# Performance work log

Hardware: AMD Instinct MI355X
Metric: run time of the kernel (lower is better)

## Reference

```python
import jax, jax.numpy as jnp
import numpy as np

B, C, H, W = 2, 256, 128, 128
QK_DIM, HEADS, TOPK, NSP = 256, 8, 128, 256
HEAD_DIM = QK_DIM // HEADS
SCALE = HEAD_DIM ** -0.5
EPS = 1e-6


def setup_inputs() -> dict:
    key = jax.random.key(0)
    ks = jax.random.split(key, 5)
    return {
        "x": jax.random.normal(ks[0], (B, C, H, W), jnp.float32),
        "affinity_matrix": jax.random.normal(ks[1], (B, NSP, H * W), jnp.float32),
        "gamma": jnp.ones((C,), jnp.float32),
        "beta": jnp.zeros((C,), jnp.float32),
        "wq": jax.random.normal(ks[2], (QK_DIM, C), jnp.float32) * 0.02,
        "wk": jax.random.normal(ks[3], (QK_DIM, C), jnp.float32) * 0.02,
        "wv": jax.random.normal(ks[4], (C, C), jnp.float32) * 0.02,
        "num_spixels": NSP,
    }


def _split_heads(a, h):
    # [B, K, T, h*c] -> [B, K, h, T, c]   (channel layout is (h c), as in the torch rearrange)
    b, k, t, d = a.shape
    return a.reshape(b, k, t, h, d // h).transpose(0, 1, 3, 2, 4)


def _merge(a):
    # 'b k h t c -> b (h c) (k t)'
    b, k, h, t, c = a.shape
    return a.transpose(0, 2, 4, 1, 3).reshape(b, h * c, k * t)


def reference(x, affinity_matrix, gamma, beta, wq, wk, wv, num_spixels):
    # LayerNorm2d: normalize over channels with eps=1e-6
    xp = x.transpose(0, 2, 3, 1)                      # [B,H,W,C]
    mu = xp.mean(-1, keepdims=True)
    var = ((xp - mu) ** 2).mean(-1, keepdims=True)
    xn = (xp - mu) / jnp.sqrt(var + EPS) * gamma + beta
    xf = xn.reshape(B, H * W, C)                      # [B, HW, C]

    # 1x1 convs == per-pixel linear
    q = xf @ wq.T                                     # [B, HW, QK]
    k = xf @ wk.T                                     # [B, HW, QK]
    v = xf @ wv.T                                     # [B, HW, C]

    sims, idx = jax.lax.top_k(affinity_matrix, TOPK)  # [B, NSP, T]

    gather = jax.vmap(lambda feat, i: feat[i])        # [HW,D],[NSP,T] -> [NSP,T,D]
    qh = _split_heads(gather(q, idx), HEADS)          # [B,K,h,T,c]
    kh = _split_heads(gather(k, idx), HEADS)
    vh = _split_heads(gather(v, idx), HEADS)

    attn = jax.nn.softmax(jnp.einsum('bkhtc,bkhsc->bkhts', qh, kh) * SCALE, axis=-1)
    w = sims[:, :, None, :, None]                     # [B,K,1,T,1]
    out = jnp.einsum('bkhts,bkhsc->bkhtc', attn, w * vh)

    out_f = _merge(out)                               # [B, C, K*T]
    w_f = _merge(jnp.broadcast_to(w, vh.shape))       # [B, C, K*T]

    tgt = v.transpose(0, 2, 1)                        # [B, C, HW]
    idx_f = idx.reshape(B, -1)                        # [B, K*T]
    scat = jax.vmap(lambda t_, i_, s_: t_.at[:, i_].add(s_))
    res = scat(tgt, idx_f, w_f * out_f)               # scatter-add over pixels
    return res.reshape(B, C, H, W)
```

## Files before the change

### kernel.cpp

```cpp
#include <hip/hip_runtime.h>
#include <hip/hip_bf16.h>

#define B_ 2
#define C_ 256
#define H_ 128
#define W_ 128
#define HW_ 16384
#define QK_ 256
#define HEADS_ 8
#define HD_ 32
#define TOPK_ 128
#define NSP_ 256
#define SCALE_F 0.17677669529663687f
#define EPS_ 1e-6f

typedef __attribute__((ext_vector_type(16))) float f32x16;
typedef __attribute__((ext_vector_type(8))) short bf16x8;
typedef unsigned short ushort_t;
union FragU { unsigned int u[4]; bf16x8 v; };

__device__ __forceinline__ ushort_t f2bf(float x)
{
    unsigned u = __float_as_uint(x);
    return (ushort_t)((u + 0x7fffu + ((u >> 16) & 1u)) >> 16);
}
__device__ __forceinline__ float bf2f(ushort_t h)
{
    return __uint_as_float((unsigned)h << 16);
}
__device__ __forceinline__ unsigned pk2(float a, float b)
{
    return (unsigned)f2bf(a) | ((unsigned)f2bf(b) << 16);
}

__device__ __forceinline__ unsigned pk2n(float a, float b)
{
    __hip_bfloat162 h2 = __float22bfloat162_rn(make_float2(a, b));
    union { __hip_bfloat162 h; unsigned u; } c;
    c.h = h2;
    return c.u;
}

__device__ __forceinline__ void half_swap(unsigned a, unsigned b,
                                          unsigned& o0, unsigned& o1, int hi)
{
#if __has_builtin(__builtin_amdgcn_permlane32_swap)
    auto r = __builtin_amdgcn_permlane32_swap(a, b, false, false);
    o0 = (unsigned)r[0];
    o1 = (unsigned)r[1];
#else
    unsigned sa = (unsigned)__shfl_xor((int)a, 32);
    unsigned sb = (unsigned)__shfl_xor((int)b, 32);
    o0 = hi ? sb : a;
    o1 = hi ? b : sa;
#endif
}

__device__ __forceinline__ size_t frag_off(int panel, int ks, int lane)
{
    return (((size_t)panel * 16 + ks) * 64 + lane) * 8;
}

__device__ __forceinline__ void split8(const float* f, FragU& hi, FragU& lo)
{
    #pragma unroll
    for (int j = 0; j < 4; j++) {
        ushort_t h0 = f2bf(f[2*j]);
        ushort_t h1 = f2bf(f[2*j+1]);
        hi.u[j] = (unsigned)h0 | ((unsigned)h1 << 16);
        lo.u[j] = pk2(f[2*j] - bf2f(h0), f[2*j+1] - bf2f(h1));
    }
}

__global__ __launch_bounds__(256) void k_meanvar(const float* __restrict__ x, float* __restrict__ mu_rstd)
{
    int p = blockIdx.x * 256 + threadIdx.x;
    int b = p >> 14, pp = p & (HW_ - 1);
    const float* xb = x + (size_t)b * C_ * HW_ + pp;
    float s = 0.f, s2 = 0.f;
    for (int c = 0; c < C_; c++) {
        float v = xb[(size_t)c * HW_];
        s += v; s2 += v * v;
    }
    float mu = s * (1.f / C_);
    float var = s2 * (1.f / C_) - mu * mu;
    float rstd = rsqrtf(var + EPS_);
    mu_rstd[2 * p] = mu;
    mu_rstd[2 * p + 1] = rstd;
}

__global__ __launch_bounds__(256) void k_wsplit16(
    const float* __restrict__ wq, const float* __restrict__ wk, const float* __restrict__ wv,
    ushort_t* __restrict__ wf)
{
    const int panel = blockIdx.x;
    const int lm = threadIdx.x & 31;
    const int kg = threadIdx.x >> 5;
    const int k0 = kg * 32;
    const int n = panel * 32 + lm;
    const float* wr = (n < 256) ? (wq + (size_t)n * C_)
                   : (n < 512) ? (wk + (size_t)(n - 256) * C_)
                               : (wv + (size_t)(n - 512) * C_);
    float v[32];
    #pragma unroll
    for (int j4 = 0; j4 < 8; j4++) {
        float4 t = *(const float4*)(wr + k0 + j4 * 4);
        v[j4*4+0] = t.x; v[j4*4+1] = t.y; v[j4*4+2] = t.z; v[j4*4+3] = t.w;
    }
    uint4 hv[4];
    unsigned* hp = (unsigned*)hv;
    #pragma unroll
    for (int jp = 0; jp < 16; jp++)
        hp[jp] = pk2n(v[2*jp], v[2*jp+1]);
    #pragma unroll
    for (int q = 0; q < 4; q++) {
        const int kk = k0 + 8 * q;
        const int ks = kk >> 4;
        const int hi = (kk >> 3) & 1;
        *(uint4*)(wf + frag_off(panel, ks, lm + 32 * hi)) = hv[q];
    }
}

__global__ __launch_bounds__(256) void k_lnsplit16(
    const float* __restrict__ x, const float* __restrict__ gamma, const float* __restrict__ beta,
    ushort_t* __restrict__ xf)
{
    const int b = blockIdx.y;
    const int m0 = blockIdx.x * 32;
    const int lm = threadIdx.x & 31;
    const int kg = threadIdx.x >> 5;
    const int k0 = kg * 32;
    const int m = m0 + lm;
    const float* xb = x + (size_t)b * C_ * HW_ + m;
    __shared__ float g_l[C_], b_l[C_];
    __shared__ float red[2][8][32];
    g_l[threadIdx.x] = gamma[threadIdx.x];
    b_l[threadIdx.x] = beta[threadIdx.x];

    float v[32];
    float s = 0.f, s2 = 0.f;
    #pragma unroll
    for (int j = 0; j < 32; j++) {
        v[j] = xb[(size_t)(k0 + j) * HW_];
        s += v[j]; s2 += v[j] * v[j];
    }
    red[0][kg][lm] = s; red[1][kg][lm] = s2;
    __syncthreads();
    float ts = 0.f, ts2 = 0.f;
    #pragma unroll
    for (int g = 0; g < 8; g++) { ts += red[0][g][lm]; ts2 += red[1][g][lm]; }
    const float mu = ts * (1.f / C_);
    const float var = ts2 * (1.f / C_) - mu * mu;
    const float rstd = rsqrtf(var + EPS_);

    uint4 hv[4];
    unsigned* hp = (unsigned*)hv;
    #pragma unroll
    for (int jp = 0; jp < 16; jp++) {
        float l0 = (v[2*jp]   - mu) * rstd * g_l[k0 + 2*jp]   + b_l[k0 + 2*jp];
        float l1 = (v[2*jp+1] - mu) * rstd * g_l[k0 + 2*jp+1] + b_l[k0 + 2*jp+1];
        hp[jp] = pk2n(l0, l1);
    }
    const int panel = b * (HW_ / 32) + blockIdx.x;
    #pragma unroll
    for (int q = 0; q < 4; q++) {
        const int kk = k0 + 8 * q;
        const int ks = kk >> 4;
        const int hi = (kk >> 3) & 1;
        *(uint4*)(xf + frag_off(panel, ks, lm + 32 * hi)) = hv[q];
    }
}

__global__ __launch_bounds__(256) void k_qkv_mfma16(
    const ushort_t* __restrict__ xf, const ushort_t* __restrict__ wf,
    ushort_t* __restrict__ qkv16)
{
    const int b = blockIdx.z;
    const int m0 = blockIdx.x * 128, n0 = blockIdx.y * 128;
    const int tid = threadIdx.x;
    const int lane = tid & 63, wv = tid >> 6;
    const int wr = wv >> 1, wc = wv & 1;
    const int lm = lane & 31;

    const int pa0 = b * (HW_ / 32) + (m0 >> 5) + wr * 2;
    const int pa1 = pa0 + 1;
    const int pb0 = (n0 >> 5) + wc * 2;
    const int pb1 = pb0 + 1;

    f32x16 acc00, acc01, acc10, acc11;
    #pragma unroll
    for (int r = 0; r < 16; r++) { acc00[r] = 0.f; acc01[r] = 0.f; acc10[r] = 0.f; acc11[r] = 0.f; }

    #pragma unroll 8
    for (int ks = 0; ks < 16; ks++) {
        bf16x8 a0 = *(const bf16x8*)(xf + frag_off(pa0, ks, lane));
        bf16x8 a1 = *(const bf16x8*)(xf + frag_off(pa1, ks, lane));
        bf16x8 b0 = *(const bf16x8*)(wf + frag_off(pb0, ks, lane));
        bf16x8 b1 = *(const bf16x8*)(wf + frag_off(pb1, ks, lane));
        acc00 = __builtin_amdgcn_mfma_f32_32x32x16_bf16(b0, a0, acc00, 0, 0, 0);
        acc01 = __builtin_amdgcn_mfma_f32_32x32x16_bf16(b1, a0, acc01, 0, 0, 0);
        acc10 = __builtin_amdgcn_mfma_f32_32x32x16_bf16(b0, a1, acc10, 0, 0, 0);
        acc11 = __builtin_amdgcn_mfma_f32_32x32x16_bf16(b1, a1, acc11, 0, 0, 0);
    }

    const int hv4 = (lane >> 5) * 4;
    #define STORE_ACC(ACC, MT, NT) { \
        ushort_t* o = qkv16 + ((size_t)b * HW_ + m0 + wr * 64 + (MT) * 32 + lm) * 768 \
                    + n0 + wc * 64 + (NT) * 32 + hv4; \
        _Pragma("unroll") \
        for (int g = 0; g < 4; g++) { \
            uint2 pr; \
            pr.x = pk2n(ACC[4*g + 0], ACC[4*g + 1]); \
            pr.y = pk2n(ACC[4*g + 2], ACC[4*g + 3]); \
            *(uint2*)(o + 8 * g) = pr; } }
    STORE_ACC(acc00, 0, 0)
    STORE_ACC(acc01, 0, 1)
    STORE_ACC(acc10, 1, 0)
    STORE_ACC(acc11, 1, 1)
    #undef STORE_ACC
}

#define GBM 128
#define GBN 128
#define GBK 8
__global__ __launch_bounds__(256) void k_qkv_gemm(
    const float* __restrict__ x, const float* __restrict__ mu_rstd,
    const float* __restrict__ gamma, const float* __restrict__ beta,
    const float* __restrict__ wq, const float* __restrict__ wk, const float* __restrict__ wv,
    float* __restrict__ qkv)
{
    const int b  = blockIdx.z;
    const int m0 = blockIdx.x * GBM;
    const int n0 = blockIdx.y * GBN;
    __shared__ float a_l[GBK][GBM + 4];
    __shared__ float b_l[GBK][GBN + 4];
    __shared__ float g_l[C_], bt_l[C_];
    const int tid = threadIdx.x;
    g_l[tid] = gamma[tid];
    bt_l[tid] = beta[tid];

    const int mm = tid & 127;
    const int kg = tid >> 7;
    const int nn = tid >> 1;
    const int kq = (tid & 1) * 4;
    const float2 mr = ((const float2*)mu_rstd)[b * HW_ + m0 + mm];
    const float* xbase = x + (size_t)b * C_ * HW_ + m0 + mm;
    const int n = n0 + nn;
    const float* wrow = (n < 256) ? (wq + (size_t)n * C_)
                     : (n < 512) ? (wk + (size_t)(n - 256) * C_)
                                 : (wv + (size_t)(n - 512) * C_);
    float acc[8][8] = {};
    const int tx = tid & 15, ty = tid >> 4;

    for (int kt = 0; kt < C_; kt += GBK) {
        __syncthreads();
        #pragma unroll
        for (int j = 0; j < 4; j++) {
            int kk = kg + j * 2;
            int c = kt + kk;
            float xv = xbase[(size_t)c * HW_];
            a_l[kk][mm] = (xv - mr.x) * mr.y * g_l[c] + bt_l[c];
        }
        float4 w4 = *(const float4*)(wrow + kt + kq);
        b_l[kq + 0][nn] = w4.x; b_l[kq + 1][nn] = w4.y;
        b_l[kq + 2][nn] = w4.z; b_l[kq + 3][nn] = w4.w;
        __syncthreads();
        #pragma unroll
        for (int kk = 0; kk < GBK; kk++) {
            float4 a0 = *(const float4*)&a_l[kk][ty * 8];
            float4 a1 = *(const float4*)&a_l[kk][ty * 8 + 4];
            float4 b0 = *(const float4*)&b_l[kk][tx * 8];
            float4 b1 = *(const float4*)&b_l[kk][tx * 8 + 4];
            float av[8] = {a0.x,a0.y,a0.z,a0.w,a1.x,a1.y,a1.z,a1.w};
            float bv[8] = {b0.x,b0.y,b0.z,b0.w,b1.x,b1.y,b1.z,b1.w};
            #pragma unroll
            for (int i = 0; i < 8; i++)
                #pragma unroll
                for (int jj = 0; jj < 8; jj++)
                    acc[i][jj] += av[i] * bv[jj];
        }
    }
    float* out0 = qkv + ((size_t)b * HW_ + m0 + ty * 8) * 768 + n0 + tx * 8;
    #pragma unroll
    for (int i = 0; i < 8; i++) {
        *(float4*)(out0 + (size_t)i * 768)     = make_float4(acc[i][0], acc[i][1], acc[i][2], acc[i][3]);
        *(float4*)(out0 + (size_t)i * 768 + 4) = make_float4(acc[i][4], acc[i][5], acc[i][6], acc[i][7]);
    }
}

__device__ __forceinline__ unsigned fkeyu(unsigned u)
{
    return (u & 0x80000000u) ? ~u : (u | 0x80000000u);
}
__device__ __forceinline__ unsigned ifkey(unsigned k)
{
    return (k & 0x80000000u) ? (k ^ 0x80000000u) : ~k;
}

__global__ __launch_bounds__(256) void k_topk(const unsigned* __restrict__ aff,
                                              int* __restrict__ idxo, float* __restrict__ simso)
{
    const int row = blockIdx.x;
    const int tid = threadIdx.x;
    const int lane = tid & 63, wid = tid >> 6;
    __shared__ __align__(16) unsigned key_l[HW_];
    __shared__ unsigned hist[8][256];
    __shared__ unsigned sh_prefix;
    __shared__ int sh_need;
    __shared__ int partG[4], partE[4];

    const uint4* a4 = (const uint4*)(aff + (size_t)row * HW_);
    #pragma unroll 4
    for (int j = 0; j < 16; j++) {
        int i4 = j * 256 + tid;
        uint4 v = a4[i4];
        key_l[4 * i4 + 0] = fkeyu(v.x);
        key_l[4 * i4 + 1] = fkeyu(v.y);
        key_l[4 * i4 + 2] = fkeyu(v.z);
        key_l[4 * i4 + 3] = fkeyu(v.w);
    }
    if (tid == 0) { sh_prefix = 0u; sh_need = TOPK_; }

    const int qbase = wid * 4096;
    const int sh_idx = wid * 2 + (lane >> 5);

    for (int pass = 0; pass < 4; pass++) {
        __syncthreads();
        #pragma unroll
        for (int z = 0; z < 8; z++) ((unsigned*)hist)[z * 256 + tid] = 0u;
        __syncthreads();
        const unsigned pref = sh_prefix;
        const unsigned need = (unsigned)sh_need;
        const int sh_hi = 32 - 8 * pass;
        const int sh_lo = sh_hi - 8;
        #pragma unroll 4
        for (int j = 0; j < 16; j++) {
            uint4 k4 = *(const uint4*)&key_l[qbase + j * 256 + lane * 4];
            #pragma unroll
            for (int e = 0; e < 4; e++) {
                unsigned key = ((const unsigned*)&k4)[e];
                if (pass == 0 || (key >> sh_hi) == pref)
                    atomicAdd(&hist[sh_idx][(key >> sh_lo) & 255u], 1u);
            }
        }
        __syncthreads();
        if (wid == 0) {
            unsigned c[4]; unsigned loc = 0;
            #pragma unroll
            for (int i = 0; i < 4; i++) {
                unsigned t = 0;
                #pragma unroll
                for (int hh = 0; hh < 8; hh++) t += hist[hh][lane*4+i];
                c[i] = t;
                loc += t;
            }
            unsigned s = loc;
            #pragma unroll
            for (int off = 1; off < 64; off <<= 1) {
                unsigned t = (unsigned)__shfl_down((int)s, off);
                if (lane + off < 64) s += t;
            }
            unsigned run = s - loc;
            #pragma unroll
            for (int i = 3; i >= 0; i--) {
                unsigned incl = run + c[i];
                if (incl >= need && run < need) {
                    sh_prefix = (pref << 8) | (unsigned)(lane * 4 + i);
                    sh_need = (int)(need - run);
                }
                run = incl;
            }
        }
    }
    __syncthreads();

    const unsigned T = sh_prefix;
    const int e_take = sh_need;

    int cg = 0, ce = 0;
    #pragma unroll 4
    for (int j = 0; j < 16; j++) {
        uint4 k4 = *(const uint4*)&key_l[qbase + j * 256 + lane * 4];
        #pragma unroll
        for (int e = 0; e < 4; e++) {
            unsigned key = ((const unsigned*)&k4)[e];
            cg += (key > T);
            ce += (key == T);
        }
    }
    #pragma unroll
    for (int o = 32; o >= 1; o >>= 1) { cg += __shfl_xor(cg, o); ce += __shfl_xor(ce, o); }
    if (lane == 0) { partG[wid] = cg; partE[wid] = ce; }
    __syncthreads();

    int gpre = 0, epre = 0;
    for (int q = 0; q < wid; q++) { gpre += partG[q]; epre += partE[q]; }
    int base = gpre + ((epre < e_take) ? epre : e_take);
    int rem_eq = e_take - epre;
    if (rem_eq < 0) rem_eq = 0;
    if (rem_eq > ce) rem_eq = ce;

    int* orow = idxo + (size_t)row * TOPK_;
    float* srow = simso + (size_t)row * TOPK_;
    const unsigned long long ltm = (1ULL << lane) - 1ULL;

    for (int j = 0; j < 64; j++) {
        const int i = qbase + j * 64 + lane;
        const unsigned key = key_l[i];
        const bool gt = key > T;
        const bool eq = (key == T);
        const unsigned long long bg = __ballot(gt);
        const unsigned long long be = __ballot(eq);
        const int cgc = __popcll(bg);
        const int cec = __popcll(be);
        if (gt) {
            int slot = base + __popcll(bg & ltm);
            orow[slot] = i; srow[slot] = __uint_as_float(ifkey(key));
        }
        if (eq && rem_eq > 0) {
            int r = __popcll(be & ltm);
            if (r < rem_eq) {
                int slot = base + cgc + r;
                orow[slot] = i; srow[slot] = __uint_as_float(ifkey(key));
            }
        }
        const int etk = (cec < rem_eq) ? cec : rem_eq;
        base += cgc + etk;
        rem_eq -= etk;
    }
}

__global__ __launch_bounds__(128) void k_count(const int* __restrict__ idxb, int* __restrict__ cnt)
{
    const int sp = blockIdx.x, b = blockIdx.y;
    int pix = idxb[(b * NSP_ + sp) * TOPK_ + threadIdx.x];
    atomicAdd(&cnt[b * HW_ + pix], 1);
}

__global__ __launch_bounds__(1024) void k_scan(const int* __restrict__ cnt, int* __restrict__ offs)
{
    const int b = blockIdx.x;
    const int tid = threadIdx.x;
    __shared__ int sc[1024];
    const int base = b * HW_;
    int loc[16];
    int s = 0;
    #pragma unroll
    for (int i = 0; i < 16; i++) {
        int c = cnt[base + tid * 16 + i];
        loc[i] = s;
        s += c;
    }
    sc[tid] = s;
    __syncthreads();
    for (int off = 1; off < 1024; off <<= 1) {
        int add = (tid >= off) ? sc[tid - off] : 0;
        __syncthreads();
        sc[tid] += add;
        __syncthreads();
    }
    int excl = sc[tid] - s;
    #pragma unroll
    for (int i = 0; i < 16; i++)
        offs[base + tid * 16 + i] = excl + loc[i];
}

__global__ __launch_bounds__(128) void k_fill(const int* __restrict__ idxb, const int* __restrict__ offs,
                                              int* __restrict__ cursor, int* __restrict__ entry)
{
    const int sp = blockIdx.x, b = blockIdx.y;
    const int slot = threadIdx.x;
    int pix = idxb[(b * NSP_ + sp) * TOPK_ + slot];
    int pos = atomicAdd(&cursor[b * HW_ + pix], 1);
    entry[b * (NSP_ * TOPK_) + offs[b * HW_ + pix] + pos] = sp * TOPK_ + slot;
}

__global__ __launch_bounds__(256, 4) void k_attn16(
    const ushort_t* __restrict__ qkv16, const int* __restrict__ idxb,
    const float* __restrict__ sims, ushort_t* __restrict__ O16)
{
    const int sp = blockIdx.x, h = blockIdx.y, b = blockIdx.z;
    __shared__ int idx_l[TOPK_];
    __shared__ float sims_l[TOPK_];
    __shared__ __align__(16) ushort_t vt[HD_][TOPK_ + 8];

    const int tid = threadIdx.x;
    const int roff = (b * NSP_ + sp) * TOPK_;
    if (tid < TOPK_) {
        idx_l[tid] = idxb[roff + tid];
        sims_l[tid] = sims[roff + tid];
    }
    __syncthreads();

    const ushort_t* qb = qkv16 + (size_t)b * HW_ * 768;

    {
        const int s = tid >> 1, ch = (tid & 1) * 16;
        const float wgt = sims_l[s];
        const ushort_t* vrow = qb + (size_t)idx_l[s] * 768 + 512 + h * HD_ + ch;
        bf16x8 v0 = *(const bf16x8*)(vrow);
        bf16x8 v1 = *(const bf16x8*)(vrow + 8);
        #pragma unroll
        for (int jp = 0; jp < 4; jp++) {
            unsigned p0 = pk2n(bf2f((ushort_t)v0[2*jp]) * wgt, bf2f((ushort_t)v0[2*jp+1]) * wgt);
            vt[ch + 2*jp][s]     = (ushort_t)p0;
            vt[ch + 2*jp + 1][s] = (ushort_t)(p0 >> 16);
            unsigned p1 = pk2n(bf2f((ushort_t)v1[2*jp]) * wgt, bf2f((ushort_t)v1[2*jp+1]) * wgt);
            vt[ch + 8 + 2*jp][s]     = (ushort_t)p1;
            vt[ch + 8 + 2*jp + 1][s] = (ushort_t)(p1 >> 16);
        }
    }

    const int lane = tid & 63, w = tid >> 6;
    const int lq = lane & 31, hi = lane >> 5;
    const int qrow = idx_l[w * 32 + lq];

    f32x16 sacc[4];
    #pragma unroll
    for (int s = 0; s < 4; s++)
        #pragma unroll
        for (int r = 0; r < 16; r++) sacc[s][r] = 0.f;

    #pragma unroll
    for (int t = 0; t < 2; t++) {
        bf16x8 qf = *(const bf16x8*)(qb + (size_t)qrow * 768 + h * HD_ + t * 16 + hi * 8);
        #pragma unroll
        for (int s = 0; s < 4; s++) {
            const int krow = idx_l[s * 32 + lq];
            bf16x8 kf = *(const bf16x8*)(qb + (size_t)krow * 768 + 256 + h * HD_ + t * 16 + hi * 8);
            sacc[s] = __builtin_amdgcn_mfma_f32_32x32x16_bf16(kf, qf, sacc[s], 0, 0, 0);
        }
    }

    float m = -1e30f;
    #pragma unroll
    for (int s = 0; s < 4; s++)
        #pragma unroll
        for (int r = 0; r < 16; r++) m = fmaxf(m, sacc[s][r]);
    m = fmaxf(m, __shfl_xor(m, 32));
    const float msc = m * SCALE_F;
    float lsum = 0.f;
    #pragma unroll
    for (int s = 0; s < 4; s++)
        #pragma unroll
        for (int r = 0; r < 16; r++) {
            float p = __expf(fmaf(sacc[s][r], SCALE_F, -msc));
            sacc[s][r] = p;
            lsum += p;
        }
    lsum += __shfl_xor(lsum, 32);

    __syncthreads();

    f32x16 oacc;
    #pragma unroll
    for (int r = 0; r < 16; r++) oacc[r] = 0.f;

    #pragma unroll
    for (int t = 0; t < 8; t++) {
        const int st = t >> 1, rb = (t & 1) * 8;
        unsigned A0 = pk2n(sacc[st][rb + 0], sacc[st][rb + 1]);
        unsigned A1 = pk2n(sacc[st][rb + 2], sacc[st][rb + 3]);
        unsigned B0 = pk2n(sacc[st][rb + 4], sacc[st][rb + 5]);
        unsigned B1 = pk2n(sacc[st][rb + 6], sacc[st][rb + 7]);
        FragU pf;
        half_swap(A0, B0, pf.u[0], pf.u[2], hi);
        half_swap(A1, B1, pf.u[1], pf.u[3], hi);
        bf16x8 vf = *(const bf16x8*)&vt[lq][t * 16 + hi * 8];
        oacc = __builtin_amdgcn_mfma_f32_32x32x16_bf16(vf, pf.v, oacc, 0, 0, 0);
    }

    const float wt = sims_l[w * 32 + lq] / lsum;
    ushort_t* orow = O16 + ((size_t)roff + w * 32 + lq) * C_ + h * HD_ + 4 * hi;
    #pragma unroll
    for (int g = 0; g < 4; g++) {
        uint2 pr;
        pr.x = pk2n(oacc[4*g + 0] * wt, oacc[4*g + 1] * wt);
        pr.y = pk2n(oacc[4*g + 2] * wt, oacc[4*g + 3] * wt);
        *(uint2*)(orow + 8 * g) = pr;
    }
}

template <bool DENSE>
__global__ __launch_bounds__(256) void k_attn_mfma(
    const float* __restrict__ qkv, const int* __restrict__ idxb,
    const float* __restrict__ sims, ushort_t* __restrict__ O16, float* __restrict__ tmp)
{
    const int sp = blockIdx.x, h = blockIdx.y, b = blockIdx.z;
    __shared__ int idx_l[TOPK_];
    __shared__ float sims_l[TOPK_];
    __shared__ __align__(16) ushort_t vt[HD_][TOPK_ + 8];

    const int tid = threadIdx.x;
    const int roff = (b * NSP_ + sp) * TOPK_;
    if (tid < TOPK_) {
        idx_l[tid] = idxb[roff + tid];
        sims_l[tid] = sims[roff + tid];
    }
    __syncthreads();

    const float* qb = qkv + (size_t)b * HW_ * 768;

    {
        const int s = tid >> 1, ch = (tid & 1) * 16;
        const float wgt = sims_l[s];
        const float* vrow = qb + (size_t)idx_l[s] * 768 + 512 + h * HD_ + ch;
        #pragma unroll
        for (int j4 = 0; j4 < 4; j4++) {
            float4 vv = *(const float4*)(vrow + j4 * 4);
            vt[ch + j4 * 4 + 0][s] = f2bf(vv.x * wgt);
            vt[ch + j4 * 4 + 1][s] = f2bf(vv.y * wgt);
            vt[ch + j4 * 4 + 2][s] = f2bf(vv.z * wgt);
            vt[ch + j4 * 4 + 3][s] = f2bf(vv.w * wgt);
        }
    }

    const int lane = tid & 63, w = tid >> 6;
    const int lq = lane & 31, hi = lane >> 5;
    const int qrow = idx_l[w * 32 + lq];

    f32x16 sacc[4];
    #pragma unroll
    for (int s = 0; s < 4; s++)
        #pragma unroll
        for (int r = 0; r < 16; r++) sacc[s][r] = 0.f;

    #pragma unroll
    for (int t = 0; t < 2; t++) {
        const float* qp = qb + (size_t)qrow * 768 + h * HD_ + t * 16 + hi * 8;
        float q8[8];
        {
            float4 t0 = *(const float4*)qp;
            float4 t1 = *(const float4*)(qp + 4);
            q8[0]=t0.x; q8[1]=t0.y; q8[2]=t0.z; q8[3]=t0.w;
            q8[4]=t1.x; q8[5]=t1.y; q8[6]=t1.z; q8[7]=t1.w;
        }
        FragU qh, ql; split8(q8, qh, ql);
        #pragma unroll
        for (int s = 0; s < 4; s++) {
            const int krow = idx_l[s * 32 + lq];
            const float* kp = qb + (size_t)krow * 768 + 256 + h * HD_ + t * 16 + hi * 8;
            float k8[8];
            {
                float4 t0 = *(const float4*)kp;
                float4 t1 = *(const float4*)(kp + 4);
                k8[0]=t0.x; k8[1]=t0.y; k8[2]=t0.z; k8[3]=t0.w;
                k8[4]=t1.x; k8[5]=t1.y; k8[6]=t1.z; k8[7]=t1.w;
            }
            FragU kh, kl; split8(k8, kh, kl);
            sacc[s] = __builtin_amdgcn_mfma_f32_32x32x16_bf16(kh.v, qh.v, sacc[s], 0, 0, 0);
            sacc[s] = __builtin_amdgcn_mfma_f32_32x32x16_bf16(kh.v, ql.v, sacc[s], 0, 0, 0);
            sacc[s] = __builtin_amdgcn_mfma_f32_32x32x16_bf16(kl.v, qh.v, sacc[s], 0, 0, 0);
        }
    }

    float m = -1e30f;
    #pragma unroll
    for (int s = 0; s < 4; s++)
        #pragma unroll
        for (int r = 0; r < 16; r++) m = fmaxf(m, sacc[s][r]);
    m = fmaxf(m, __shfl_xor(m, 32));
    float lsum = 0.f;
    #pragma unroll
    for (int s = 0; s < 4; s++)
        #pragma unroll
        for (int r = 0; r < 16; r++) {
            float p = __expf((sacc[s][r] - m) * SCALE_F);
            sacc[s][r] = p;
            lsum += p;
        }
    lsum += __shfl_xor(lsum, 32);

    __syncthreads();

    f32x16 oacc;
    #pragma unroll
    for (int r = 0; r < 16; r++) oacc[r] = 0.f;

    #pragma unroll
    for (int t = 0; t < 8; t++) {
        const int st = t >> 1, rb = (t & 1) * 8;
        unsigned A0 = pk2(sacc[st][rb + 0], sacc[st][rb + 1]);
        unsigned A1 = pk2(sacc[st][rb + 2], sacc[st][rb + 3]);
        unsigned B0 = pk2(sacc[st][rb + 4], sacc[st][rb + 5]);
        unsigned B1 = pk2(sacc[st][rb + 6], sacc[st][rb + 7]);
        unsigned sA0 = (unsigned)__shfl_xor((int)A0, 32);
        unsigned sA1 = (unsigned)__shfl_xor((int)A1, 32);
        unsigned sB0 = (unsigned)__shfl_xor((int)B0, 32);
        unsigned sB1 = (unsigned)__shfl_xor((int)B1, 32);
        FragU pf;
        pf.u[0] = hi ? sB0 : A0;
        pf.u[1] = hi ? sB1 : A1;
        pf.u[2] = hi ? B0 : sA0;
        pf.u[3] = hi ? B1 : sA1;
        bf16x8 vf = *(const bf16x8*)&vt[lq][t * 16 + hi * 8];
        oacc = __builtin_amdgcn_mfma_f32_32x32x16_bf16(vf, pf.v, oacc, 0, 0, 0);
    }

    const float wt = sims_l[w * 32 + lq] / lsum;
    if (DENSE) {
        ushort_t* orow = O16 + ((size_t)roff + w * 32 + lq) * C_ + h * HD_ + 4 * hi;
        #pragma unroll
        for (int g = 0; g < 4; g++) {
            uint2 pr;
            pr.x = pk2(oacc[4*g + 0] * wt, oacc[4*g + 1] * wt);
            pr.y = pk2(oacc[4*g + 2] * wt, oacc[4*g + 3] * wt);
            *(uint2*)(orow + 8 * g) = pr;
        }
    } else {
        float* drow = tmp + ((size_t)(b * HW_) + qrow) * C_ + h * HD_;
        #pragma unroll
        for (int r = 0; r < 16; r++) {
            int c = (r & 3) + 8 * (r >> 2) + 4 * hi;
            atomicAdd(&drow[c], oacc[r] * wt);
        }
    }
}

__global__ __launch_bounds__(128) void k_attn_fb(
    const float* __restrict__ qkv, const int* __restrict__ idxb,
    const float* __restrict__ sims, float* __restrict__ dst)
{
    const int sp = blockIdx.x, h = blockIdx.y, b = blockIdx.z;
    __shared__ float k_l[TOPK_][HD_];
    __shared__ float vw_l[TOPK_][HD_];
    __shared__ float sims_l[TOPK_];
    __shared__ int idx_l[TOPK_];
    const int tid = threadIdx.x;
    const int roff = (b * NSP_ + sp) * TOPK_;
    idx_l[tid] = idxb[roff + tid];
    sims_l[tid] = sims[roff + tid];
    __syncthreads();
    const float* base = qkv + (size_t)b * HW_ * 768;
    #pragma unroll
    for (int it = 0; it < 8; it++) {
        int flat = it * 128 + tid;
        int s = flat >> 3, c4 = (flat & 7) * 4;
        const float* krow = base + (size_t)idx_l[s] * 768 + 256 + h * HD_ + c4;
        *(float4*)&k_l[s][c4] = *(const float4*)krow;
        const float* vrow = base + (size_t)idx_l[s] * 768 + 512 + h * HD_ + c4;
        float4 vv = *(const float4*)vrow;
        float wgt = sims_l[s];
        *(float4*)&vw_l[s][c4] = make_float4(vv.x * wgt, vv.y * wgt, vv.z * wgt, vv.w * wgt);
    }
    float q[HD_];
    const int pix = idx_l[tid];
    const float* qrow = base + (size_t)pix * 768 + h * HD_;
    #pragma unroll
    for (int j = 0; j < 8; j++) {
        float4 t4 = *(const float4*)(qrow + j * 4);
        q[j*4] = t4.x; q[j*4+1] = t4.y; q[j*4+2] = t4.z; q[j*4+3] = t4.w;
    }
    __syncthreads();
    float m = -1e30f, l = 0.f, acc[HD_];
    #pragma unroll
    for (int c = 0; c < HD_; c++) acc[c] = 0.f;
    for (int s = 0; s < TOPK_; s++) {
        float d = 0.f;
        #pragma unroll
        for (int c4 = 0; c4 < 8; c4++) {
            float4 kk4 = *(const float4*)&k_l[s][c4 * 4];
            d += q[c4*4]*kk4.x + q[c4*4+1]*kk4.y + q[c4*4+2]*kk4.z + q[c4*4+3]*kk4.w;
        }
        d *= SCALE_F;
        float mn = fmaxf(m, d);
        float fac = __expf(m - mn);
        float p = __expf(d - mn);
        l = l * fac + p;
        #pragma unroll
        for (int c4 = 0; c4 < 8; c4++) {
            float4 vv4 = *(const float4*)&vw_l[s][c4 * 4];
            acc[c4*4]   = acc[c4*4]   * fac + p * vv4.x;
            acc[c4*4+1] = acc[c4*4+1] * fac + p * vv4.y;
            acc[c4*4+2] = acc[c4*4+2] * fac + p * vv4.z;
            acc[c4*4+3] = acc[c4*4+3] * fac + p * vv4.w;
        }
        m = mn;
    }
    const float wt = sims_l[tid] / l;
    float* dbase = dst + ((size_t)b * C_ + h * HD_) * HW_ + pix;
    #pragma unroll
    for (int c = 0; c < HD_; c++) atomicAdd(dbase + (size_t)c * HW_, acc[c] * wt);
}

__global__ __launch_bounds__(256) void k_final216(
    const ushort_t* __restrict__ qkv16, const ushort_t* __restrict__ O16,
    const int* __restrict__ cnt, const int* __restrict__ offs,
    const int* __restrict__ entry, float* __restrict__ out)
{
    const int b = blockIdx.z;
    const int p0 = blockIdx.x * 64, c0 = blockIdx.y * 64;
    __shared__ float t[64][65];
    const int tid = threadIdx.x;
    const int cc = tid & 63;
    #pragma unroll
    for (int it = 0; it < 16; it++) {
        int r = it * 4 + (tid >> 6);
        int p = p0 + r;
        float val = bf2f(qkv16[((size_t)b * HW_ + p) * 768 + 512 + c0 + cc]);
        int n = cnt[b * HW_ + p];
        const int* ep = entry + b * (NSP_ * TOPK_) + offs[b * HW_ + p];
        for (int j = 0; j < n; j++) {
            int e = ep[j];
            val += bf2f(O16[((size_t)b * (NSP_ * TOPK_) + e) * C_ + c0 + cc]);
        }
        t[r][cc] = val;
    }
    __syncthreads();
    #pragma unroll
    for (int it = 0; it < 16; it++) {
        int flat = it * 256 + tid;
        int rr = flat >> 6, pp = flat & 63;
        out[((size_t)b * C_ + c0 + rr) * HW_ + p0 + pp] = t[pp][rr];
    }
}

__global__ __launch_bounds__(256) void k_final2(
    const float* __restrict__ qkv, const ushort_t* __restrict__ O16,
    const int* __restrict__ cnt, const int* __restrict__ offs,
    const int* __restrict__ entry, float* __restrict__ out)
{
    const int b = blockIdx.z;
    const int p0 = blockIdx.x * 64, c0 = blockIdx.y * 64;
    __shared__ float t[64][65];
    const int tid = threadIdx.x;
    const int cc = tid & 63;
    #pragma unroll
    for (int it = 0; it < 16; it++) {
        int r = it * 4 + (tid >> 6);
        int p = p0 + r;
        float val = qkv[((size_t)b * HW_ + p) * 768 + 512 + c0 + cc];
        int n = cnt[b * HW_ + p];
        const int* ep = entry + b * (NSP_ * TOPK_) + offs[b * HW_ + p];
        for (int j = 0; j < n; j++) {
            int e = ep[j];
            val += bf2f(O16[((size_t)b * (NSP_ * TOPK_) + e) * C_ + c0 + cc]);
        }
        t[r][cc] = val;
    }
    __syncthreads();
    #pragma unroll
    for (int it = 0; it < 16; it++) {
        int flat = it * 256 + tid;
        int rr = flat >> 6, pp = flat & 63;
        out[((size_t)b * C_ + c0 + rr) * HW_ + p0 + pp] = t[pp][rr];
    }
}

__global__ __launch_bounds__(256) void k_final(const float* __restrict__ qkv,
                                               const float* __restrict__ tmp, float* __restrict__ out)
{
    const int b = blockIdx.z;
    const int p0 = blockIdx.x * 64, c0 = blockIdx.y * 64;
    __shared__ float t[64][65];
    const int tid = threadIdx.x;
    #pragma unroll
    for (int it = 0; it < 16; it++) {
        int flat = it * 256 + tid;
        int r = flat >> 6, cc2 = flat & 63;
        float v = qkv[((size_t)b * HW_ + p0 + r) * 768 + 512 + c0 + cc2]
                + tmp[((size_t)b * HW_ + p0 + r) * C_ + c0 + cc2];
        t[r][cc2] = v;
    }
    __syncthreads();
    #pragma unroll
    for (int it = 0; it < 16; it++) {
        int flat = it * 256 + tid;
        int rr = flat >> 6, pp = flat & 63;
        out[((size_t)b * C_ + c0 + rr) * HW_ + p0 + pp] = t[pp][rr];
    }
}

__global__ __launch_bounds__(256) void k_vinit(const float* __restrict__ qkv, float* __restrict__ out)
{
    const int b = blockIdx.z;
    const int p0 = blockIdx.x * 64, c0 = blockIdx.y * 64;
    __shared__ float t[64][65];
    const int tid = threadIdx.x;
    #pragma unroll
    for (int it = 0; it < 16; it++) {
        int flat = it * 256 + tid;
        int r = flat >> 6, cc2 = flat & 63;
        t[r][cc2] = qkv[((size_t)b * HW_ + p0 + r) * 768 + 512 + c0 + cc2];
    }
    __syncthreads();
    #pragma unroll
    for (int it = 0; it < 16; it++) {
        int flat = it * 256 + tid;
        int rr = flat >> 6, pp = flat & 63;
        out[((size_t)b * C_ + c0 + rr) * HW_ + p0 + pp] = t[pp][rr];
    }
}

extern "C" void kernel_launch(void* const* d_in, const int* in_sizes, int n_in,
                              void* d_out, int out_size, void* d_ws, size_t ws_size,
                              hipStream_t stream)
{
    (void)in_sizes; (void)n_in; (void)out_size;
    const float* x     = (const float*)d_in[0];
    const float* aff   = (const float*)d_in[1];
    const float* gamma = (const float*)d_in[2];
    const float* beta  = (const float*)d_in[3];
    const float* wq    = (const float*)d_in[4];
    const float* wk    = (const float*)d_in[5];
    const float* wv    = (const float*)d_in[6];
    float* out = (float*)d_out;
    float* ws  = (float*)d_ws;

    const size_t n_mu   = (size_t)2 * B_ * HW_;
    const size_t n_qkv  = (size_t)B_ * HW_ * 768;
    const size_t n_idx  = (size_t)B_ * NSP_ * TOPK_;
    const size_t n_o16  = (size_t)B_ * NSP_ * TOPK_ * C_ / 2;
    const size_t n_pix  = (size_t)B_ * HW_;
    const size_t n_w2f  = (size_t)768 * C_;
    const size_t n_tmp  = (size_t)B_ * HW_ * C_;

    float*    mu_rstd = ws;
    float*    qkv     = ws + n_mu;
    ushort_t* qkv16   = (ushort_t*)(ws + n_mu);
    int*      idxb    = (int*)(ws + n_mu + n_qkv);
    float*    sims    = ws + n_mu + n_qkv + n_idx;
    float*    big     = ws + n_mu + n_qkv + 2 * n_idx;
    ushort_t* O16     = (ushort_t*)big;
    ushort_t* xf      = (ushort_t*)big;
    int*      cnt     = (int*)(big + n_o16);
    int*      offs    = cnt + n_pix;
    int*      cursor  = offs + n_pix;
    int*      entry   = cursor + n_pix;
    ushort_t* wf      = (ushort_t*)(entry + n_idx);

    const size_t need_t1  = (n_mu + n_qkv + 2 * n_idx + n_o16 + 3 * n_pix + n_idx + n_w2f) * 4;
    const size_t need_t2  = (n_mu + n_qkv + 2 * n_idx + n_o16 + 3 * n_pix + n_idx) * 4;
    const size_t need_mid = (n_mu + n_qkv + 2 * n_idx + n_tmp) * 4;

    if (ws_size >= need_t1) {
        k_wsplit16<<<dim3(24), 256, 0, stream>>>(wq, wk, wv, wf);
        k_lnsplit16<<<dim3(HW_ / 32, B_), 256, 0, stream>>>(x, gamma, beta, xf);
        k_qkv_mfma16<<<dim3(HW_ / 128, 768 / 128, B_), 256, 0, stream>>>(xf, wf, qkv16);
        k_topk<<<dim3(B_ * NSP_), 256, 0, stream>>>((const unsigned*)aff, idxb, sims);
        hipMemsetAsync(cnt, 0, 3 * n_pix * 4, stream);
        dim3 gsp(NSP_, B_);
        k_count<<<gsp, 128, 0, stream>>>(idxb, cnt);
        k_scan<<<dim3(B_), 1024, 0, stream>>>(cnt, offs);
        k_fill<<<gsp, 128, 0, stream>>>(idxb, offs, cursor, entry);
        dim3 ga(NSP_, HEADS_, B_);
        k_attn16<<<ga, 256, 0, stream>>>(qkv16, idxb, sims, O16);
        dim3 gf(HW_ / 64, C_ / 64, B_);
        k_final216<<<gf, 256, 0, stream>>>(qkv16, O16, cnt, offs, entry, out);
    } else if (ws_size >= need_t2) {
        k_meanvar<<<dim3((B_ * HW_) / 256), 256, 0, stream>>>(x, mu_rstd);
        dim3 gg(HW_ / GBM, 768 / GBN, B_);
        k_qkv_gemm<<<gg, 256, 0, stream>>>(x, mu_rstd, gamma, beta, wq, wk, wv, qkv);
        k_topk<<<dim3(B_ * NSP_), 256, 0, stream>>>((const unsigned*)aff, idxb, sims);
        hipMemsetAsync(cnt, 0, 3 * n_pix * 4, stream);
        dim3 gsp(NSP_, B_);
        k_count<<<gsp, 128, 0, stream>>>(idxb, cnt);
        k_scan<<<dim3(B_), 1024, 0, stream>>>(cnt, offs);
        k_fill<<<gsp, 128, 0, stream>>>(idxb, offs, cursor, entry);
        dim3 ga(NSP_, HEADS_, B_);
        k_attn_mfma<true><<<ga, 256, 0, stream>>>(qkv, idxb, sims, O16, nullptr);
        dim3 gf(HW_ / 64, C_ / 64, B_);
        k_final2<<<gf, 256, 0, stream>>>(qkv, O16, cnt, offs, entry, out);
    } else if (ws_size >= need_mid) {
        k_meanvar<<<dim3((B_ * HW_) / 256), 256, 0, stream>>>(x, mu_rstd);
        dim3 gg(HW_ / GBM, 768 / GBN, B_);
        k_qkv_gemm<<<gg, 256, 0, stream>>>(x, mu_rstd, gamma, beta, wq, wk, wv, qkv);
        k_topk<<<dim3(B_ * NSP_), 256, 0, stream>>>((const unsigned*)aff, idxb, sims);
        float* tmp = big;
        hipMemsetAsync(tmp, 0, n_tmp * 4, stream);
        dim3 ga(NSP_, HEADS_, B_);
        k_attn_mfma<false><<<ga, 256, 0, stream>>>(qkv, idxb, sims, nullptr, tmp);
        dim3 gf(HW_ / 64, C_ / 64, B_);
        k_final<<<gf, 256, 0, stream>>>(qkv, tmp, out);
    } else {
        k_meanvar<<<dim3((B_ * HW_) / 256), 256, 0, stream>>>(x, mu_rstd);
        dim3 gg(HW_ / GBM, 768 / GBN, B_);
        k_qkv_gemm<<<gg, 256, 0, stream>>>(x, mu_rstd, gamma, beta, wq, wk, wv, qkv);
        k_topk<<<dim3(B_ * NSP_), 256, 0, stream>>>((const unsigned*)aff, idxb, sims);
        dim3 gf(HW_ / 64, C_ / 64, B_);
        k_vinit<<<gf, 256, 0, stream>>>(qkv, out);
        dim3 ga(NSP_, HEADS_, B_);
        k_attn_fb<<<ga, 128, 0, stream>>>(qkv, idxb, sims, out);
    }
}
```

Before: 173.9 us.

## Compact radix-select candidates into shared buffer after first top-k pass

The radix-select top-k kernel now gathers the keys that share the current winning prefix into a small shared candidate buffer once that bucket fits (up to 896 entries). Later histogram passes then scan only the candidates instead of all 16384 keys in LDS. Per-pass histogram clearing and the prefix logic are restructured around this. The change adds shared memory, extra barriers and atomic-counter compaction, and falls back to the full scan when the bucket is too large.

Result: no change. 173.6 us, median of 4 (-0.2%).

```diff
diff --git a/kernel.cpp b/kernel.cpp
--- a/kernel.cpp
+++ b/kernel.cpp
@@ -13,6 +13,7 @@
 #define NSP_ 256
 #define SCALE_F 0.17677669529663687f
 #define EPS_ 1e-6f
+#define CAP_ 896
 
 typedef __attribute__((ext_vector_type(16))) float f32x16;
 typedef __attribute__((ext_vector_type(8))) short bf16x8;
@@ -305,7 +306,8 @@
     const int lane = tid & 63, wid = tid >> 6;
     __shared__ __align__(16) unsigned key_l[HW_];
     __shared__ unsigned hist[8][256];
-    __shared__ unsigned sh_prefix;
+    __shared__ unsigned cand[2][CAP_];
+    __shared__ unsigned sh_prefix, sh_E, sh_cnt;
     __shared__ int sh_need;
     __shared__ int partG[4], partE[4];
 
@@ -319,32 +321,30 @@
         key_l[4 * i4 + 2] = fkeyu(v.z);
         key_l[4 * i4 + 3] = fkeyu(v.w);
     }
+    #pragma unroll
+    for (int z = 0; z < 8; z++) ((unsigned*)hist)[z * 256 + tid] = 0u;
     if (tid == 0) { sh_prefix = 0u; sh_need = TOPK_; }
+    __syncthreads();
 
     const int qbase = wid * 4096;
     const int sh_idx = wid * 2 + (lane >> 5);
 
+    #pragma unroll 4
+    for (int j = 0; j < 16; j++) {
+        uint4 k4 = *(const uint4*)&key_l[qbase + j * 256 + lane * 4];
+        #pragma unroll
+        for (int e = 0; e < 4; e++)
+            atomicAdd(&hist[sh_idx][((const unsigned*)&k4)[e] >> 24], 1u);
+    }
+    __syncthreads();
+
+    bool compacted = false;
+    int cur = 0, Ecur = 0;
+
     for (int pass = 0; pass < 4; pass++) {
-        __syncthreads();
-        #pragma unroll
-        for (int z = 0; z < 8; z++) ((unsigned*)hist)[z * 256 + tid] = 0u;
-        __syncthreads();
-        const unsigned pref = sh_prefix;
-        const unsigned need = (unsigned)sh_need;
-        const int sh_hi = 32 - 8 * pass;
-        const int sh_lo = sh_hi - 8;
-        #pragma unroll 4
-        for (int j = 0; j < 16; j++) {
-            uint4 k4 = *(const uint4*)&key_l[qbase + j * 256 + lane * 4];
-            #pragma unroll
-            for (int e = 0; e < 4; e++) {
-                unsigned key = ((const unsigned*)&k4)[e];
-                if (pass == 0 || (key >> sh_hi) == pref)
-                    atomicAdd(&hist[sh_idx][(key >> sh_lo) & 255u], 1u);
-            }
-        }
-        __syncthreads();
         if (wid == 0) {
+            const unsigned pref = sh_prefix;
+            const unsigned need = (unsigned)sh_need;
             unsigned c[4]; unsigned loc = 0;
             #pragma unroll
             for (int i = 0; i < 4; i++) {
@@ -367,12 +367,64 @@
                 if (incl >= need && run < need) {
                     sh_prefix = (pref << 8) | (unsigned)(lane * 4 + i);
                     sh_need = (int)(need - run);
+                    sh_E = c[i];
                 }
                 run = incl;
             }
         }
-    }
-    __syncthreads();
+        __syncthreads();
+        if (pass == 3) break;
+
+        const unsigned prefT = sh_prefix;
+        const int winnerE = (int)sh_E;
+        const int shift = 24 - 8 * pass;
+        const bool do_cf = (!compacted && winnerE <= CAP_);
+        if (tid == 0) sh_cnt = 0u;
+        __syncthreads();
+
+        if (do_cf) {
+            #pragma unroll 4
+            for (int j = 0; j < 16; j++) {
+                uint4 k4 = *(const uint4*)&key_l[qbase + j * 256 + lane * 4];
+                #pragma unroll
+                for (int e = 0; e < 4; e++) {
+                    unsigned key = ((const unsigned*)&k4)[e];
+                    if ((key >> shift) == prefT)
+                        cand[0][atomicAdd(&sh_cnt, 1u)] = key;
+                }
+            }
+        } else if (compacted) {
+            for (int i = tid; i < Ecur; i += 256) {
+                unsigned key = cand[cur][i];
+                if ((key >> shift) == prefT)
+                    cand[cur ^ 1][atomicAdd(&sh_cnt, 1u)] = key;
+            }
+        }
+        __syncthreads();
+        if (do_cf) { compacted = true; cur = 0; Ecur = winnerE; }
+        else if (compacted) { cur ^= 1; Ecur = winnerE; }
+
+        #pragma unroll
+        for (int z = 0; z < 8; z++) ((unsigned*)hist)[z * 256 + tid] = 0u;
+        __syncthreads();
+        const int nshift = shift - 8;
+        if (compacted) {
+            for (int i = tid; i < Ecur; i += 256)
+                atomicAdd(&hist[sh_idx][(cand[cur][i] >> nshift) & 255u], 1u);
+        } else {
+            #pragma unroll 4
+            for (int j = 0; j < 16; j++) {
+                uint4 k4 = *(const uint4*)&key_l[qbase + j * 256 + lane * 4];
+                #pragma unroll
+                for (int e = 0; e < 4; e++) {
+                    unsigned key = ((const unsigned*)&k4)[e];
+                    if ((key >> shift) == prefT)
+                        atomicAdd(&hist[sh_idx][(key >> nshift) & 255u], 1u);
+                }
+            }
+        }
+        __syncthreads();
+    }
 
     const unsigned T = sh_prefix;
     const int e_take = sh_need;
```
